# Optimization experiments

Hardware: AMD Instinct MI355X
Metric: run time of the kernel (lower is better)

Reference implementation:

```python
import jax, jax.numpy as jnp
import numpy as np

ALPHA = 1.0


def setup_inputs() -> dict:
    key = jax.random.key(0)
    k1, k2 = jax.random.split(key)
    N, D, K = 262144, 256, 256
    x = jax.random.normal(k1, (N, D), dtype=jnp.float32)
    clusters = jax.random.normal(k2, (K, D), dtype=jnp.float32)
    return {"x": x, "clusters": clusters}


def reference(x, clusters):
    # Squared euclidean distance to each cluster center without materializing
    x_sq = jnp.sum(x * x, axis=1, keepdims=True)            # (N, 1)
    c_sq = jnp.sum(clusters * clusters, axis=1)[None, :]    # (1, K)
    cross = jnp.einsum('nd,kd->nk', x, clusters)            # (N, K)
    sq_dist = x_sq - 2.0 * cross + c_sq                     # (N, K)
    # Student-t kernel (as in t-SNE / DEC): q_ij = (1 + d^2/alpha)^(-(alpha+1)/2)
    q = 1.0 / (1.0 + sq_dist / ALPHA)
    q = q ** ((ALPHA + 1.0) / 2.0)
    # Row-normalize to soft assignment probabilities.
    q = q / jnp.sum(q, axis=1, keepdims=True)
    return q
```

## Files before the change

kernel.cpp:

```cpp
#include <hip/hip_runtime.h>


#define NROWS 262144
#define DDIM  256
#define KCL   256
#define TPB   16
#define GRID  (NROWS / 64 / TPB)

using f32x4  = __attribute__((ext_vector_type(4))) float;
using s16x8  = __attribute__((ext_vector_type(8))) short;

__device__ inline unsigned short f2bf(float f) {
    unsigned int u = __float_as_uint(f);
    u += 0x7fffu + ((u >> 16) & 1u);
    return (unsigned short)(u >> 16);
}

__global__ void prep_kernel(const float* __restrict__ clusters,
                            unsigned short* __restrict__ cb,
                            float* __restrict__ csq) {
    int k    = blockIdx.x;
    int lane = threadIdx.x;
    const float* row = clusters + (size_t)k * DDIM;
    float4 a = *reinterpret_cast<const float4*>(row + lane * 4);
    ushort4 b;
    b.x = f2bf(a.x); b.y = f2bf(a.y); b.z = f2bf(a.z); b.w = f2bf(a.w);
    *reinterpret_cast<ushort4*>(cb + (size_t)k * DDIM + lane * 4) = b;
    float ss = a.x*a.x + a.y*a.y + a.z*a.z + a.w*a.w;
    #pragma unroll
    for (int m = 1; m < 64; m <<= 1) ss += __shfl_xor(ss, m);
    if (lane == 0) csq[k] = ss;
}

__global__ __launch_bounds__(512, 2) void fused_kernel(
    const float* __restrict__ x,
    const unsigned short* __restrict__ cb,
    const float* __restrict__ csq,
    float* __restrict__ out) {

    __shared__ char  lds_b[KCL * DDIM * 2];
    __shared__ float ls_sum[2][2][4][16];

    const int tid  = threadIdx.x;
    const int lane = tid & 63;
    const int wave = tid >> 6;
    const int rg   = wave >> 1;
    const int ch   = wave & 1;
    const int c15  = lane & 15;
    const int kch  = lane >> 4;

    const int tile0 = blockIdx.x * TPB;

    #pragma unroll
    for (int it = 0; it < 16; ++it) {
        int slot = it * 8192 + tid * 16;
        int src  = slot ^ (((slot >> 9) & 7) << 4);
        __builtin_amdgcn_global_load_lds(
            (const __attribute__((address_space(1))) unsigned int*)((const char*)cb + src),
            (__attribute__((address_space(3))) unsigned int*)(lds_b + slot),
            16, 0, 0);
    }

    float cs[8];
    #pragma unroll
    for (int f = 0; f < 8; ++f) cs[f] = csq[ch * 128 + f * 16 + c15];

    __syncthreads();

    #pragma unroll 1
    for (int t = 0; t < TPB; ++t) {
        const int trow = (tile0 + t) * 64;
        const float* xrow =
            x + (size_t)(trow + rg * 16 + c15) * DDIM + kch * 8;

        s16x8 afrag[8];
        float xsq;
        {
            float p[4] = {0.f, 0.f, 0.f, 0.f};
            #pragma unroll
            for (int h = 0; h < 2; ++h) {
                f32x4 xv[8];
                #pragma unroll
                for (int i = 0; i < 8; ++i) {
                    int ii = h * 8 + i;
                    xv[i] = *reinterpret_cast<const f32x4*>(xrow + (ii >> 1) * 32 + (ii & 1) * 4);
                }
                #pragma unroll
                for (int s4 = 0; s4 < 4; ++s4) {
                    int s = h * 4 + s4;
                    f32x4 xa = xv[2 * s4], xb = xv[2 * s4 + 1];
                    float t0 = xa[0]*xa[0] + xa[1]*xa[1];
                    float t1 = xa[2]*xa[2] + xa[3]*xa[3];
                    float t2 = xb[0]*xb[0] + xb[1]*xb[1];
                    float t3 = xb[2]*xb[2] + xb[3]*xb[3];
                    p[s & 3] += (t0 + t1) + (t2 + t3);
                    afrag[s][0] = (short)f2bf(xa[0]); afrag[s][1] = (short)f2bf(xa[1]);
                    afrag[s][2] = (short)f2bf(xa[2]); afrag[s][3] = (short)f2bf(xa[3]);
                    afrag[s][4] = (short)f2bf(xb[0]); afrag[s][5] = (short)f2bf(xb[1]);
                    afrag[s][6] = (short)f2bf(xb[2]); afrag[s][7] = (short)f2bf(xb[3]);
                }
            }
            xsq = (p[0] + p[1]) + (p[2] + p[3]);
        }

        f32x4 acc[8];
        #pragma unroll
        for (int f = 0; f < 8; ++f) acc[f] = (f32x4){0.f, 0.f, 0.f, 0.f};

        #pragma unroll
        for (int s = 0; s < 8; ++s) {
            #pragma unroll
            for (int f = 0; f < 8; ++f) {
                int ba = ((ch * 128 + f * 16 + c15) * 512) + s * 64 + kch * 16;
                ba ^= ((c15 & 7) << 4);
                s16x8 bfrag = *reinterpret_cast<const s16x8*>(lds_b + ba);
                acc[f] = __builtin_amdgcn_mfma_f32_16x16x32_bf16(afrag[s], bfrag,
                                                                 acc[f], 0, 0, 0);
            }
        }

        xsq += __shfl_xor(xsq, 16);
        xsq += __shfl_xor(xsq, 32);

        float psum[4];
        #pragma unroll
        for (int r = 0; r < 4; ++r) {
            float xr = __shfl(xsq, kch * 4 + r);
            float s = 0.f;
            #pragma unroll
            for (int f = 0; f < 8; ++f) {
                float d2 = xr - 2.0f * acc[f][r] + cs[f];
                float qv = 1.0f / (1.0f + d2);
                acc[f][r] = qv;
                s += qv;
            }
            s += __shfl_xor(s, 1);
            s += __shfl_xor(s, 2);
            s += __shfl_xor(s, 4);
            s += __shfl_xor(s, 8);
            psum[r] = s;
        }

        if (c15 == 0) {
            #pragma unroll
            for (int r = 0; r < 4; ++r)
                ls_sum[t & 1][ch][rg][kch * 4 + r] = psum[r];
        }
        __syncthreads();

        const int row0t = trow + rg * 16;
        #pragma unroll
        for (int r = 0; r < 4; ++r) {
            float other = ls_sum[t & 1][ch ^ 1][rg][kch * 4 + r];
            float inv = 1.0f / (psum[r] + other);
            const size_t orow = (size_t)(row0t + kch * 4 + r) * KCL;
            #pragma unroll
            for (int f = 0; f < 8; ++f) {
                __builtin_nontemporal_store(acc[f][r] * inv,
                                            &out[orow + ch * 128 + f * 16 + c15]);
            }
        }
    }
}

extern "C" void kernel_launch(void* const* d_in, const int* in_sizes, int n_in,
                              void* d_out, int out_size, void* d_ws, size_t ws_size,
                              hipStream_t stream) {
    const float* x        = (const float*)d_in[0];
    const float* clusters = (const float*)d_in[1];
    float* out = (float*)d_out;

    unsigned short* cb  = (unsigned short*)d_ws;
    float*          csq = (float*)((char*)d_ws + (size_t)KCL * DDIM * sizeof(unsigned short));

    prep_kernel<<<KCL, 64, 0, stream>>>(clusters, cb, csq);
    fused_kernel<<<GRID, 512, 0, stream>>>(x, cb, csq, out);
}
```

Before: 135.5 us.

## Prefetch next x tile across MFMA and replace block barrier with pairwise LDS flags

Splits the x load into two halves: the second half is loaded while MFMAs run on the first, and the first half of the next tile is prefetched during the second MFMA pass, so global latency hides behind matrix math. The per-tile __syncthreads is replaced by a pairwise LDS flag handshake between the two waves sharing a row group, with ls_sum indexed per tile to avoid reuse hazards. Divisions are replaced by hardware rcp approximations. This adds register pressure (two 8-vector x buffers), relies on a spin-wait with relaxed ordering that could be fragile, and the approximate reciprocal slightly changes numerics.

```diff
diff --git a/kernel.cpp b/kernel.cpp
--- a/kernel.cpp
+++ b/kernel.cpp
@@ -39,7 +39,8 @@
     float* __restrict__ out) {
 
     __shared__ char  lds_b[KCL * DDIM * 2];
-    __shared__ float ls_sum[2][2][4][16];
+    __shared__ float ls_sum[TPB][2][4][16];
+    __shared__ int   ls_flag[2][4];
 
     const int tid  = threadIdx.x;
     const int lane = tid & 63;
@@ -61,46 +62,53 @@
             16, 0, 0);
     }
 
+    if (tid < 8) ((int*)ls_flag)[tid] = 0;
+
     float cs[8];
     #pragma unroll
     for (int f = 0; f < 8; ++f) cs[f] = csq[ch * 128 + f * 16 + c15];
 
     __syncthreads();
 
+    auto xrow = [&](int t) -> const float* {
+        return x + (size_t)((tile0 + t) * 64 + rg * 16 + c15) * DDIM + kch * 8;
+    };
+
+    f32x4 xv1[8], xv2[8];
+
+    {
+        const float* xr = xrow(0);
+        #pragma unroll
+        for (int i = 0; i < 8; ++i)
+            xv1[i] = *reinterpret_cast<const f32x4*>(xr + (i >> 1) * 32 + (i & 1) * 4);
+    }
+
     #pragma unroll 1
     for (int t = 0; t < TPB; ++t) {
         const int trow = (tile0 + t) * 64;
-        const float* xrow =
-            x + (size_t)(trow + rg * 16 + c15) * DDIM + kch * 8;
+        const float* xr = xrow(t);
 
         s16x8 afrag[8];
-        float xsq;
-        {
-            float p[4] = {0.f, 0.f, 0.f, 0.f};
-            #pragma unroll
-            for (int h = 0; h < 2; ++h) {
-                f32x4 xv[8];
-                #pragma unroll
-                for (int i = 0; i < 8; ++i) {
-                    int ii = h * 8 + i;
-                    xv[i] = *reinterpret_cast<const f32x4*>(xrow + (ii >> 1) * 32 + (ii & 1) * 4);
-                }
-                #pragma unroll
-                for (int s4 = 0; s4 < 4; ++s4) {
-                    int s = h * 4 + s4;
-                    f32x4 xa = xv[2 * s4], xb = xv[2 * s4 + 1];
-                    float t0 = xa[0]*xa[0] + xa[1]*xa[1];
-                    float t1 = xa[2]*xa[2] + xa[3]*xa[3];
-                    float t2 = xb[0]*xb[0] + xb[1]*xb[1];
-                    float t3 = xb[2]*xb[2] + xb[3]*xb[3];
-                    p[s & 3] += (t0 + t1) + (t2 + t3);
-                    afrag[s][0] = (short)f2bf(xa[0]); afrag[s][1] = (short)f2bf(xa[1]);
-                    afrag[s][2] = (short)f2bf(xa[2]); afrag[s][3] = (short)f2bf(xa[3]);
-                    afrag[s][4] = (short)f2bf(xb[0]); afrag[s][5] = (short)f2bf(xb[1]);
-                    afrag[s][6] = (short)f2bf(xb[2]); afrag[s][7] = (short)f2bf(xb[3]);
-                }
-            }
-            xsq = (p[0] + p[1]) + (p[2] + p[3]);
+        float p[4] = {0.f, 0.f, 0.f, 0.f};
+
+        #pragma unroll
+        for (int s4 = 0; s4 < 4; ++s4) {
+            f32x4 xa = xv1[2 * s4], xb = xv1[2 * s4 + 1];
+            float t0 = xa[0]*xa[0] + xa[1]*xa[1];
+            float t1 = xa[2]*xa[2] + xa[3]*xa[3];
+            float t2 = xb[0]*xb[0] + xb[1]*xb[1];
+            float t3 = xb[2]*xb[2] + xb[3]*xb[3];
+            p[s4] += (t0 + t1) + (t2 + t3);
+            afrag[s4][0] = (short)f2bf(xa[0]); afrag[s4][1] = (short)f2bf(xa[1]);
+            afrag[s4][2] = (short)f2bf(xa[2]); afrag[s4][3] = (short)f2bf(xa[3]);
+            afrag[s4][4] = (short)f2bf(xb[0]); afrag[s4][5] = (short)f2bf(xb[1]);
+            afrag[s4][6] = (short)f2bf(xb[2]); afrag[s4][7] = (short)f2bf(xb[3]);
+        }
+
+        #pragma unroll
+        for (int i = 0; i < 8; ++i) {
+            int ii = 8 + i;
+            xv2[i] = *reinterpret_cast<const f32x4*>(xr + (ii >> 1) * 32 + (ii & 1) * 4);
         }
 
         f32x4 acc[8];
@@ -108,7 +116,7 @@
         for (int f = 0; f < 8; ++f) acc[f] = (f32x4){0.f, 0.f, 0.f, 0.f};
 
         #pragma unroll
-        for (int s = 0; s < 8; ++s) {
+        for (int s = 0; s < 4; ++s) {
             #pragma unroll
             for (int f = 0; f < 8; ++f) {
                 int ba = ((ch * 128 + f * 16 + c15) * 512) + s * 64 + kch * 16;
@@ -119,18 +127,53 @@
             }
         }
 
+        #pragma unroll
+        for (int s4 = 0; s4 < 4; ++s4) {
+            f32x4 xa = xv2[2 * s4], xb = xv2[2 * s4 + 1];
+            float t0 = xa[0]*xa[0] + xa[1]*xa[1];
+            float t1 = xa[2]*xa[2] + xa[3]*xa[3];
+            float t2 = xb[0]*xb[0] + xb[1]*xb[1];
+            float t3 = xb[2]*xb[2] + xb[3]*xb[3];
+            p[s4] += (t0 + t1) + (t2 + t3);
+            int s = 4 + s4;
+            afrag[s][0] = (short)f2bf(xa[0]); afrag[s][1] = (short)f2bf(xa[1]);
+            afrag[s][2] = (short)f2bf(xa[2]); afrag[s][3] = (short)f2bf(xa[3]);
+            afrag[s][4] = (short)f2bf(xb[0]); afrag[s][5] = (short)f2bf(xb[1]);
+            afrag[s][6] = (short)f2bf(xb[2]); afrag[s][7] = (short)f2bf(xb[3]);
+        }
+
+        #pragma unroll
+        for (int s = 4; s < 8; ++s) {
+            #pragma unroll
+            for (int f = 0; f < 8; ++f) {
+                int ba = ((ch * 128 + f * 16 + c15) * 512) + s * 64 + kch * 16;
+                ba ^= ((c15 & 7) << 4);
+                s16x8 bfrag = *reinterpret_cast<const s16x8*>(lds_b + ba);
+                acc[f] = __builtin_amdgcn_mfma_f32_16x16x32_bf16(afrag[s], bfrag,
+                                                                 acc[f], 0, 0, 0);
+            }
+        }
+
+        if (t + 1 < TPB) {
+            const float* xn = xrow(t + 1);
+            #pragma unroll
+            for (int i = 0; i < 8; ++i)
+                xv1[i] = *reinterpret_cast<const f32x4*>(xn + (i >> 1) * 32 + (i & 1) * 4);
+        }
+
+        float xsq = (p[0] + p[1]) + (p[2] + p[3]);
         xsq += __shfl_xor(xsq, 16);
         xsq += __shfl_xor(xsq, 32);
 
         float psum[4];
         #pragma unroll
         for (int r = 0; r < 4; ++r) {
-            float xr = __shfl(xsq, kch * 4 + r);
+            float xrr = __shfl(xsq, kch * 4 + r);
             float s = 0.f;
             #pragma unroll
             for (int f = 0; f < 8; ++f) {
-                float d2 = xr - 2.0f * acc[f][r] + cs[f];
-                float qv = 1.0f / (1.0f + d2);
+                float d2 = xrr - 2.0f * acc[f][r] + cs[f];
+                float qv = __builtin_amdgcn_rcpf(1.0f + d2);
                 acc[f][r] = qv;
                 s += qv;
             }
@@ -144,15 +187,21 @@
         if (c15 == 0) {
             #pragma unroll
             for (int r = 0; r < 4; ++r)
-                ls_sum[t & 1][ch][rg][kch * 4 + r] = psum[r];
-        }
-        __syncthreads();
+                ls_sum[t][ch][rg][kch * 4 + r] = psum[r];
+        }
+        asm volatile("s_waitcnt lgkmcnt(0)" ::: "memory");
+        if (lane == 0)
+            __atomic_store_n(&ls_flag[ch][rg], t + 1, __ATOMIC_RELAXED);
+
+        volatile int* pf = (volatile int*)&ls_flag[ch ^ 1][rg];
+        while (*pf <= t) { }
+        asm volatile("" ::: "memory");
 
         const int row0t = trow + rg * 16;
         #pragma unroll
         for (int r = 0; r < 4; ++r) {
-            float other = ls_sum[t & 1][ch ^ 1][rg][kch * 4 + r];
-            float inv = 1.0f / (psum[r] + other);
+            float other = ls_sum[t][ch ^ 1][rg][kch * 4 + r];
+            float inv = __builtin_amdgcn_rcpf(psum[r] + other);
             const size_t orow = (size_t)(row0t + kch * 4 + r) * KCL;
             #pragma unroll
             for (int f = 0; f < 8; ++f) {
```

New measurement: 131.1 us. 1.03x faster.

## Software-pipeline x loads across two row tiles with pairwise wave flag sync

Applied to the files above, without the earlier changes.

Restructures the fused kernel so each wave pair processes two 16-row strips at once, prefetching the next half of x into registers while MFMAs run on the current half. Block-wide __syncthreads is replaced by a per-pair LDS flag spin-wait, cluster norms move to LDS, and exact reciprocals become hardware rcp approximations. The aim is to hide global load latency and remove barrier stalls. In exchange it raises register pressure and uses a spin-wait whose memory ordering is fragile.

```diff
diff --git a/kernel.cpp b/kernel.cpp
--- a/kernel.cpp
+++ b/kernel.cpp
@@ -1,11 +1,14 @@
 #include <hip/hip_runtime.h>
+#include <hip/hip_bf16.h>
 
 
 #define NROWS 262144
 #define DDIM  256
 #define KCL   256
-#define TPB   16
-#define GRID  (NROWS / 64 / TPB)
+#define GRID  256
+#define PPB   4
+#define NPAIRS (GRID * PPB)
+#define NSUPER 8
 
 using f32x4  = __attribute__((ext_vector_type(4))) float;
 using s16x8  = __attribute__((ext_vector_type(8))) short;
@@ -14,6 +17,10 @@
     unsigned int u = __float_as_uint(f);
     u += 0x7fffu + ((u >> 16) & 1u);
     return (unsigned short)(u >> 16);
+}
+
+__device__ inline short bfc(float f) {
+    return (short)__bfloat16_as_ushort(__float2bfloat16(f));
 }
 
 __global__ void prep_kernel(const float* __restrict__ clusters,
@@ -39,7 +46,9 @@
     float* __restrict__ out) {
 
     __shared__ char  lds_b[KCL * DDIM * 2];
-    __shared__ float ls_sum[2][2][4][16];
+    __shared__ float ls_csq[KCL];
+    __shared__ float ls_sum[2][2][2][PPB][16];
+    __shared__ int   ls_flag[2][PPB];
 
     const int tid  = threadIdx.x;
     const int lane = tid & 63;
@@ -49,7 +58,7 @@
     const int c15  = lane & 15;
     const int kch  = lane >> 4;
 
-    const int tile0 = blockIdx.x * TPB;
+    const int g = blockIdx.x * PPB + rg;
 
     #pragma unroll
     for (int it = 0; it < 16; ++it) {
@@ -60,106 +69,145 @@
             (__attribute__((address_space(3))) unsigned int*)(lds_b + slot),
             16, 0, 0);
     }
-
-    float cs[8];
-    #pragma unroll
-    for (int f = 0; f < 8; ++f) cs[f] = csq[ch * 128 + f * 16 + c15];
+    if (tid < KCL) ls_csq[tid] = csq[tid];
+    if (tid < 2 * PPB) ((int*)ls_flag)[tid] = 0;
+
+    auto xbase = [&](int sid) -> const float* {
+        return x + (size_t)(sid * 16 + c15) * DDIM + kch * 8;
+    };
+    auto loadhalf = [&](f32x4* xv, const float* base) {
+        #pragma unroll
+        for (int i = 0; i < 8; ++i)
+            xv[i] = *reinterpret_cast<const f32x4*>(base + (i >> 1) * 32 + (i & 1) * 4);
+    };
+
+    f32x4 xvA[8], xvB[8];
+    loadhalf(xvA, xbase(g));
+    loadhalf(xvB, xbase(g + NPAIRS));
 
     __syncthreads();
 
+    auto convhalf = [&](const f32x4* xv, s16x8* af, float& q0, float& q1) {
+        #pragma unroll
+        for (int s4 = 0; s4 < 4; ++s4) {
+            f32x4 xa = xv[2 * s4], xb = xv[2 * s4 + 1];
+            float t0 = xa[0]*xa[0] + xa[1]*xa[1];
+            float t1 = xa[2]*xa[2] + xa[3]*xa[3];
+            float t2 = xb[0]*xb[0] + xb[1]*xb[1];
+            float t3 = xb[2]*xb[2] + xb[3]*xb[3];
+            if (s4 & 1) q1 += (t0 + t1) + (t2 + t3);
+            else        q0 += (t0 + t1) + (t2 + t3);
+            af[s4][0] = bfc(xa[0]); af[s4][1] = bfc(xa[1]);
+            af[s4][2] = bfc(xa[2]); af[s4][3] = bfc(xa[3]);
+            af[s4][4] = bfc(xb[0]); af[s4][5] = bfc(xb[1]);
+            af[s4][6] = bfc(xb[2]); af[s4][7] = bfc(xb[3]);
+        }
+    };
+
     #pragma unroll 1
-    for (int t = 0; t < TPB; ++t) {
-        const int trow = (tile0 + t) * 64;
-        const float* xrow =
-            x + (size_t)(trow + rg * 16 + c15) * DDIM + kch * 8;
-
-        s16x8 afrag[8];
-        float xsq;
-        {
-            float p[4] = {0.f, 0.f, 0.f, 0.f};
-            #pragma unroll
-            for (int h = 0; h < 2; ++h) {
-                f32x4 xv[8];
-                #pragma unroll
-                for (int i = 0; i < 8; ++i) {
-                    int ii = h * 8 + i;
-                    xv[i] = *reinterpret_cast<const f32x4*>(xrow + (ii >> 1) * 32 + (ii & 1) * 4);
-                }
-                #pragma unroll
-                for (int s4 = 0; s4 < 4; ++s4) {
-                    int s = h * 4 + s4;
-                    f32x4 xa = xv[2 * s4], xb = xv[2 * s4 + 1];
-                    float t0 = xa[0]*xa[0] + xa[1]*xa[1];
-                    float t1 = xa[2]*xa[2] + xa[3]*xa[3];
-                    float t2 = xb[0]*xb[0] + xb[1]*xb[1];
-                    float t3 = xb[2]*xb[2] + xb[3]*xb[3];
-                    p[s & 3] += (t0 + t1) + (t2 + t3);
-                    afrag[s][0] = (short)f2bf(xa[0]); afrag[s][1] = (short)f2bf(xa[1]);
-                    afrag[s][2] = (short)f2bf(xa[2]); afrag[s][3] = (short)f2bf(xa[3]);
-                    afrag[s][4] = (short)f2bf(xb[0]); afrag[s][5] = (short)f2bf(xb[1]);
-                    afrag[s][6] = (short)f2bf(xb[2]); afrag[s][7] = (short)f2bf(xb[3]);
-                }
-            }
-            xsq = (p[0] + p[1]) + (p[2] + p[3]);
-        }
-
-        f32x4 acc[8];
-        #pragma unroll
-        for (int f = 0; f < 8; ++f) acc[f] = (f32x4){0.f, 0.f, 0.f, 0.f};
-
-        #pragma unroll
-        for (int s = 0; s < 8; ++s) {
+    for (int j = 0; j < NSUPER; ++j) {
+        const int sA = g + 2 * NPAIRS * j;
+        const int sB = sA + NPAIRS;
+        const float* xrA = xbase(sA);
+        const float* xrB = xbase(sB);
+
+        s16x8 afA[4], afB[4];
+        float pA0 = 0.f, pA1 = 0.f, pB0 = 0.f, pB1 = 0.f;
+
+        convhalf(xvA, afA, pA0, pA1);
+        loadhalf(xvA, xrA + 128);
+        convhalf(xvB, afB, pB0, pB1);
+        loadhalf(xvB, xrB + 128);
+
+        f32x4 accA[8], accB[8];
+        #pragma unroll
+        for (int f = 0; f < 8; ++f) {
+            accA[f] = (f32x4){0.f, 0.f, 0.f, 0.f};
+            accB[f] = (f32x4){0.f, 0.f, 0.f, 0.f};
+        }
+
+        #pragma unroll
+        for (int s = 0; s < 4; ++s) {
             #pragma unroll
             for (int f = 0; f < 8; ++f) {
                 int ba = ((ch * 128 + f * 16 + c15) * 512) + s * 64 + kch * 16;
                 ba ^= ((c15 & 7) << 4);
                 s16x8 bfrag = *reinterpret_cast<const s16x8*>(lds_b + ba);
-                acc[f] = __builtin_amdgcn_mfma_f32_16x16x32_bf16(afrag[s], bfrag,
-                                                                 acc[f], 0, 0, 0);
-            }
-        }
-
-        xsq += __shfl_xor(xsq, 16);
-        xsq += __shfl_xor(xsq, 32);
-
-        float psum[4];
-        #pragma unroll
-        for (int r = 0; r < 4; ++r) {
-            float xr = __shfl(xsq, kch * 4 + r);
-            float s = 0.f;
+                accA[f] = __builtin_amdgcn_mfma_f32_16x16x32_bf16(afA[s], bfrag,
+                                                                  accA[f], 0, 0, 0);
+                accB[f] = __builtin_amdgcn_mfma_f32_16x16x32_bf16(afB[s], bfrag,
+                                                                  accB[f], 0, 0, 0);
+            }
+        }
+
+        convhalf(xvA, afA, pA0, pA1);
+        if (j + 1 < NSUPER) loadhalf(xvA, xbase(sA + 2 * NPAIRS));
+        convhalf(xvB, afB, pB0, pB1);
+        if (j + 1 < NSUPER) loadhalf(xvB, xbase(sB + 2 * NPAIRS));
+
+        #pragma unroll
+        for (int s = 0; s < 4; ++s) {
             #pragma unroll
             for (int f = 0; f < 8; ++f) {
-                float d2 = xr - 2.0f * acc[f][r] + cs[f];
-                float qv = 1.0f / (1.0f + d2);
-                acc[f][r] = qv;
-                s += qv;
-            }
-            s += __shfl_xor(s, 1);
-            s += __shfl_xor(s, 2);
-            s += __shfl_xor(s, 4);
-            s += __shfl_xor(s, 8);
-            psum[r] = s;
-        }
-
-        if (c15 == 0) {
-            #pragma unroll
-            for (int r = 0; r < 4; ++r)
-                ls_sum[t & 1][ch][rg][kch * 4 + r] = psum[r];
-        }
-        __syncthreads();
-
-        const int row0t = trow + rg * 16;
-        #pragma unroll
-        for (int r = 0; r < 4; ++r) {
-            float other = ls_sum[t & 1][ch ^ 1][rg][kch * 4 + r];
-            float inv = 1.0f / (psum[r] + other);
-            const size_t orow = (size_t)(row0t + kch * 4 + r) * KCL;
-            #pragma unroll
-            for (int f = 0; f < 8; ++f) {
-                __builtin_nontemporal_store(acc[f][r] * inv,
-                                            &out[orow + ch * 128 + f * 16 + c15]);
-            }
-        }
+                int ba = ((ch * 128 + f * 16 + c15) * 512) + (s + 4) * 64 + kch * 16;
+                ba ^= ((c15 & 7) << 4);
+                s16x8 bfrag = *reinterpret_cast<const s16x8*>(lds_b + ba);
+                accA[f] = __builtin_amdgcn_mfma_f32_16x16x32_bf16(afA[s], bfrag,
+                                                                  accA[f], 0, 0, 0);
+                accB[f] = __builtin_amdgcn_mfma_f32_16x16x32_bf16(afB[s], bfrag,
+                                                                  accB[f], 0, 0, 0);
+            }
+        }
+
+        float psA[4], psB[4];
+        auto epi = [&](f32x4* acc, float p0, float p1, float* ps, int ab) {
+            float xsq = p0 + p1;
+            xsq += __shfl_xor(xsq, 16);
+            xsq += __shfl_xor(xsq, 32);
+            #pragma unroll
+            for (int r = 0; r < 4; ++r) {
+                float xrr = __shfl(xsq, kch * 4 + r);
+                float s = 0.f;
+                #pragma unroll
+                for (int f = 0; f < 8; ++f) {
+                    float d2 = xrr - 2.0f * acc[f][r] + ls_csq[ch * 128 + f * 16 + c15];
+                    float qv = __builtin_amdgcn_rcpf(1.0f + d2);
+                    acc[f][r] = qv;
+                    s += qv;
+                }
+                s += __shfl_xor(s, 1);
+                s += __shfl_xor(s, 2);
+                s += __shfl_xor(s, 4);
+                s += __shfl_xor(s, 8);
+                ps[r] = s;
+                if (c15 == 0) ls_sum[j & 1][ab][ch][rg][kch * 4 + r] = s;
+            }
+        };
+        epi(accA, pA0, pA1, psA, 0);
+        epi(accB, pB0, pB1, psB, 1);
+
+        asm volatile("s_waitcnt lgkmcnt(0)" ::: "memory");
+        if (lane == 0)
+            __atomic_store_n(&ls_flag[ch][rg], j + 1, __ATOMIC_RELAXED);
+        volatile int* pf = (volatile int*)&ls_flag[ch ^ 1][rg];
+        while (*pf <= j) { }
+        asm volatile("" ::: "memory");
+
+        auto dostores = [&](f32x4* acc, const float* ps, int ab, int sid) {
+            #pragma unroll
+            for (int r = 0; r < 4; ++r) {
+                float other = ls_sum[j & 1][ab][ch ^ 1][rg][kch * 4 + r];
+                float inv = __builtin_amdgcn_rcpf(ps[r] + other);
+                const size_t orow = (size_t)(sid * 16 + kch * 4 + r) * KCL;
+                #pragma unroll
+                for (int f = 0; f < 8; ++f) {
+                    __builtin_nontemporal_store(acc[f][r] * inv,
+                                                &out[orow + ch * 128 + f * 16 + c15]);
+                }
+            }
+        };
+        dostores(accA, psA, 0, sA);
+        dostores(accB, psB, 1, sB);
     }
 }
 
```

Result: slower. 289.5 us (+113.6%).
